# Kernel optimization log

Hardware: AMD Instinct MI355X
Metric: run time of the kernel (lower is better)

## Reference

```python
import jax, jax.numpy as jnp
import numpy as np

B, S, H = 4, 2048, 512
E, K = 8, 2
DFF = 4 * H


def setup_inputs() -> dict:
    key = jax.random.key(0)
    ks = jax.random.split(key, 6)
    x = jax.random.normal(ks[0], (B, S, H), dtype=jnp.float32)
    gate_W = jax.random.normal(ks[1], (H, E), dtype=jnp.float32) * 0.02
    gate_b = jnp.zeros((E,), dtype=jnp.float32)
    # Stacked expert params; Linear stored as [in, out] so y = x @ W + b
    W1 = jax.random.normal(ks[2], (E, H, DFF), dtype=jnp.float32) * 0.02
    b1 = jnp.zeros((E, DFF), dtype=jnp.float32)
    W2 = jax.random.normal(ks[3], (E, DFF, H), dtype=jnp.float32) * 0.02
    b2 = jnp.zeros((E, H), dtype=jnp.float32)
    return {"x": x, "gate_W": gate_W, "gate_b": gate_b,
            "W1": W1, "b1": b1, "W2": W2, "b2": b2}


def reference(x, gate_W, gate_b, W1, b1, W2, b2):
    bsz, seq, hid = x.shape
    flat = x.reshape(-1, hid)                       # [T, H]
    T = flat.shape[0]
    gate_logits = flat @ gate_W + gate_b            # [T, E]
    topk_vals, topk_idx = jax.lax.top_k(gate_logits, K)   # [T, K]
    topk_w = jax.nn.softmax(topk_vals, axis=-1)      # softmax over selected logits only

    # Scatter top-k weights into a dense per-token combine matrix [T, E];
    # zero weight where a token is not routed -> identical math to masked dispatch.
    combine = jnp.zeros((T, E), dtype=flat.dtype).at[
        jnp.arange(T)[:, None], topk_idx].add(topk_w)

    out_flat = jnp.zeros_like(flat)
    for e in range(E):  # fixed small loop over structurally distinct experts
        h = jax.nn.gelu(flat @ W1[e] + b1[e], approximate=False) @ W2[e] + b2[e]
        out_flat = out_flat + h * combine[:, e:e + 1]
    out = out_flat.reshape(bsz, seq, hid)

    probs = jax.nn.softmax(gate_logits, axis=-1).mean(axis=0)   # [E]
    l_aux = jnp.sum(probs * probs) * E
    expert_counts = jnp.zeros((E,), dtype=jnp.float32).at[
        topk_idx.reshape(-1)].add(1.0)
    return out, l_aux, expert_counts
```

## Files before the change

kernel.cpp:

```cpp
#include <hip/hip_runtime.h>
#include <math.h>

#define TOK 8192
#define HD  512
#define NE  8
#define DFF 2048

typedef __attribute__((ext_vector_type(8))) short bf16x8;
typedef __attribute__((ext_vector_type(4))) float floatx4;

__device__ inline unsigned short f2bf(float f) {
    union { float f; unsigned u; } v; v.f = f;
    unsigned r = v.u + 0x7FFFu + ((v.u >> 16) & 1u);
    return (unsigned short)(r >> 16);
}

__device__ inline float gelu_exact(float v) {
    return 0.5f * v * (1.f + erff(v * 0.70710678118654752f));
}

typedef __attribute__((address_space(1))) const unsigned int glb_u32;
typedef __attribute__((address_space(3))) unsigned int lds_u32;
__device__ __forceinline__ void gload16(const unsigned short* g, unsigned short* l) {
    __builtin_amdgcn_global_load_lds((glb_u32*)g, (lds_u32*)l, 16, 0, 0);
}

__global__ __launch_bounds__(256) void prep_kernel(
    const float* __restrict__ x, const float* __restrict__ gW, const float* __restrict__ gb,
    const float* __restrict__ W1, const float* __restrict__ W2,
    int* __restrict__ seg_count, float* __restrict__ probs_sum,
    int* __restrict__ seg_token, float* __restrict__ seg_w,
    unsigned short* __restrict__ xb,
    unsigned short* __restrict__ W1t, unsigned short* __restrict__ W2t)
{
    __shared__ __align__(16) char shraw[16896];
    int bid = blockIdx.x;
    int tid = threadIdx.x;

    if (bid >= 32) {
        int b = bid - 32;
        float (*tile)[65] = (float(*)[65])shraw;
        int z = b >> 8, rem = b & 255;
        int xq = rem & 31, yq = rem >> 5;
        const float* src; unsigned short* dst; int C, R, cb, rb;
        if (z < NE) {
            src = W1 + (size_t)z * HD * DFF; dst = W1t + (size_t)z * HD * DFF;
            R = HD; C = DFF; cb = xq; rb = yq;
        } else {
            int e = z - NE;
            src = W2 + (size_t)e * DFF * HD; dst = W2t + (size_t)e * DFF * HD;
            R = DFF; C = HD; cb = yq; rb = xq;
        }
        int c0 = cb * 64, r0 = rb * 64;
        int lc = tid & 63, lrw = tid >> 6;
        #pragma unroll
        for (int rr = lrw; rr < 64; rr += 4)
            tile[rr][lc] = src[(size_t)(r0 + rr) * C + c0 + lc];
        __syncthreads();
        #pragma unroll
        for (int cc = lrw; cc < 64; cc += 4)
            dst[(size_t)(c0 + cc) * R + r0 + lc] = f2bf(tile[lc][cc]);
        return;
    }

    float* sW    = (float*)shraw;
    float* psum  = (float*)(shraw + 16384);
    int*   lcount = (int*)(shraw + 16448);
    int*   lbase  = (int*)(shraw + 16512);

    for (int i = tid; i < HD * NE; i += 256) sW[i] = gW[i];
    if (tid < NE) { psum[tid] = 0.f; lcount[tid] = 0; }
    __syncthreads();

    int t = bid * 256 + tid;
    float logit[NE];
    #pragma unroll
    for (int e = 0; e < NE; e++) logit[e] = gb[e];

    const float4* xr4 = reinterpret_cast<const float4*>(x + (size_t)t * HD);
    ushort4* xbw = reinterpret_cast<ushort4*>(xb + (size_t)t * HD);
    for (int j4 = 0; j4 < HD / 4; j4++) {
        float4 xv = xr4[j4];
        int j = j4 * 4;
        ushort4 o; o.x = f2bf(xv.x); o.y = f2bf(xv.y); o.z = f2bf(xv.z); o.w = f2bf(xv.w);
        xbw[j4] = o;
        #pragma unroll
        for (int e = 0; e < NE; e++) {
            logit[e] += xv.x * sW[(j + 0) * NE + e] + xv.y * sW[(j + 1) * NE + e]
                      + xv.z * sW[(j + 2) * NE + e] + xv.w * sW[(j + 3) * NE + e];
        }
    }

    float mx = logit[0];
    #pragma unroll
    for (int e = 1; e < NE; e++) mx = fmaxf(mx, logit[e]);
    float pe[NE]; float s = 0.f;
    #pragma unroll
    for (int e = 0; e < NE; e++) { pe[e] = expf(logit[e] - mx); s += pe[e]; }
    float inv = 1.f / s;
    int l = tid & 63;
    #pragma unroll
    for (int e = 0; e < NE; e++) {
        float v = pe[e] * inv;
        for (int off = 32; off; off >>= 1) v += __shfl_down(v, off);
        if (l == 0) atomicAdd(&psum[e], v);
    }

    int i0 = 0; float v0 = logit[0];
    #pragma unroll
    for (int e = 1; e < NE; e++) if (logit[e] > v0) { v0 = logit[e]; i0 = e; }
    int i1 = -1; float v1 = -3.4e38f;
    #pragma unroll
    for (int e = 0; e < NE; e++) if (e != i0 && logit[e] > v1) { v1 = logit[e]; i1 = e; }
    float e1 = expf(v1 - v0);
    float w0 = 1.f / (1.f + e1);
    float w1 = e1 / (1.f + e1);

    int r0 = atomicAdd(&lcount[i0], 1);
    int r1 = atomicAdd(&lcount[i1], 1);
    __syncthreads();
    if (tid < NE) lbase[tid] = atomicAdd(&seg_count[tid], lcount[tid]);
    __syncthreads();
    int p0 = lbase[i0] + r0;
    seg_token[i0 * TOK + p0] = t; seg_w[i0 * TOK + p0] = w0;
    int p1 = lbase[i1] + r1;
    seg_token[i1 * TOK + p1] = t; seg_w[i1 * TOK + p1] = w1;

    __syncthreads();
    if (tid < NE) atomicAdd(&probs_sum[tid], psum[tid]);
}

#define TM  128
#define TN  128
#define BK  32

__global__ __launch_bounds__(256) void gemm1_kernel(
    const unsigned short* __restrict__ xb,
    const unsigned short* __restrict__ W1t,
    const float* __restrict__ bias1,
    const int* __restrict__ seg_count, const float* __restrict__ probs_sum,
    const int* __restrict__ seg_token,
    unsigned short* __restrict__ hbuf,
    float* __restrict__ out_tail)
{
    int bid = blockIdx.x;
    int tid = threadIdx.x;

    if (bid == 0) {
        if (tid < NE) out_tail[1 + tid] = (float)seg_count[tid];
        else if (tid == 64) {
            float s = 0.f;
            #pragma unroll
            for (int e2 = 0; e2 < NE; e2++) {
                float p = probs_sum[e2] * (1.f / (float)TOK);
                s += p * p;
            }
            out_tail[0] = s * (float)NE;
        }
    }

    int e  = bid & 7;
    int r2 = bid >> 3;
    int nb = r2 & 15;
    int mb = r2 >> 4;
    int cnt = seg_count[e];
    if (mb * TM >= cnt) return;
    int off_e = 0;
    #pragma unroll
    for (int ee = 0; ee < NE; ee++) if (ee < e) off_e += (seg_count[ee] + 127) & ~127;
    int hb = off_e + mb * TM;

    __shared__ __align__(16) unsigned short smem[3][2][TM * BK];
    __shared__ int tok_s[TM];
    if (tid < TM) {
        int gi = mb * TM + tid;
        tok_s[tid] = seg_token[e * TOK + ((gi < cnt) ? gi : 0)];
    }
    __syncthreads();

    int w = tid >> 6, l = tid & 63;
    int lr = l & 15, crow = (l >> 4) * 4;
    int wm = (w & 1) * 64, wn = (w >> 1) * 64;
    int kq = (l >> 4) * 8;
    const unsigned short* w1e = W1t + (size_t)e * DFF * HD + (size_t)(nb * TN) * HD;

    unsigned aofs[2], bofs[2];
    #pragma unroll
    for (int s = 0; s < 2; s++) {
        int r = w * 32 + s * 16 + (l >> 2);
        aofs[s] = (unsigned)tok_s[r] * HD + (unsigned)((l & 3) * 8);
        bofs[s] = (unsigned)(r * HD) + (unsigned)((l & 3) * 8);
    }

    floatx4 acc[4][4];
    #pragma unroll
    for (int i = 0; i < 4; i++)
        #pragma unroll
        for (int j = 0; j < 4; j++) acc[i][j] = (floatx4){0.f, 0.f, 0.f, 0.f};

    #pragma unroll
    for (int p = 0; p < 2; p++)
        #pragma unroll
        for (int s = 0; s < 2; s++) {
            gload16(xb  + aofs[s] + p * BK, &smem[p][0][(w * 32 + s * 16) * BK]);
            gload16(w1e + bofs[s] + p * BK, &smem[p][1][(w * 32 + s * 16) * BK]);
        }

    const int NIT = HD / BK;
    int rb = 0;
    for (int k = 0; k < NIT; ++k) {
        if (k + 1 < NIT) asm volatile("s_waitcnt vmcnt(4)" ::: "memory");
        else             asm volatile("s_waitcnt vmcnt(0)" ::: "memory");
        __builtin_amdgcn_s_barrier();
        asm volatile("" ::: "memory");
        if (k + 2 < NIT) {
            int ib = (rb == 0) ? 2 : rb - 1;
            int ko = (k + 2) * BK;
            #pragma unroll
            for (int s = 0; s < 2; s++) {
                gload16(xb  + aofs[s] + ko, &smem[ib][0][(w * 32 + s * 16) * BK]);
                gload16(w1e + bofs[s] + ko, &smem[ib][1][(w * 32 + s * 16) * BK]);
            }
        }
        const unsigned short* A = smem[rb][0];
        const unsigned short* B = smem[rb][1];
        bf16x8 a[4], b[4];
        #pragma unroll
        for (int i = 0; i < 4; i++) a[i] = *(const bf16x8*)&A[(wm + 16 * i + lr) * BK + kq];
        #pragma unroll
        for (int j = 0; j < 4; j++) b[j] = *(const bf16x8*)&B[(wn + 16 * j + lr) * BK + kq];
        __builtin_amdgcn_s_setprio(1);
        #pragma unroll
        for (int i = 0; i < 4; i++)
            #pragma unroll
            for (int j = 0; j < 4; j++)
                acc[i][j] = __builtin_amdgcn_mfma_f32_16x16x32_bf16(a[i], b[j], acc[i][j], 0, 0, 0);
        __builtin_amdgcn_s_setprio(0);
        rb = (rb == 2) ? 0 : rb + 1;
    }
    __syncthreads();

    unsigned short* scr = &smem[0][0][0] + w * 64 * 72;
    #pragma unroll
    for (int j = 0; j < 4; j++) {
        float b1v = bias1[e * DFF + nb * TN + wn + 16 * j + lr];
        #pragma unroll
        for (int i = 0; i < 4; i++)
            #pragma unroll
            for (int rr = 0; rr < 4; rr++)
                scr[(16 * i + crow + rr) * 72 + 16 * j + lr] = f2bf(gelu_exact(acc[i][j][rr] + b1v));
    }
    __syncthreads();
    int lh = l >> 3, ll = l & 7;
    #pragma unroll
    for (int k = 0; k < 8; k++) {
        uint4 v = *(const uint4*)&scr[(8 * k + lh) * 72 + ll * 8];
        int grow = hb + wm + 8 * k + lh;
        *(uint4*)&hbuf[(size_t)grow * DFF + nb * TN + wn + ll * 8] = v;
    }
}

__global__ __launch_bounds__(256) void gemm2_kernel(
    const unsigned short* __restrict__ hbuf,
    const unsigned short* __restrict__ W2t,
    const float* __restrict__ b2,
    const int* __restrict__ seg_count, const int* __restrict__ seg_token,
    const float* __restrict__ seg_w,
    float* __restrict__ out)
{
    int bid = blockIdx.x;
    int tid = threadIdx.x;
    int e  = bid & 7;
    int r2 = bid >> 3;
    int nb = r2 & 3;
    int mb = r2 >> 2;
    int cnt = seg_count[e];
    if (mb * TM >= cnt) return;
    int off_e = 0;
    #pragma unroll
    for (int ee = 0; ee < NE; ee++) if (ee < e) off_e += (seg_count[ee] + 127) & ~127;
    int hb = off_e + mb * TM;

    __shared__ __align__(16) unsigned short smem[3][2][TM * BK];
    __shared__ int   tok_s[TM];
    __shared__ float wgt_s[TM];
    if (tid < TM) {
        int gi = mb * TM + tid;
        tok_s[tid] = seg_token[e * TOK + ((gi < cnt) ? gi : 0)];
        wgt_s[tid] = (gi < cnt) ? seg_w[e * TOK + gi] : 0.f;
    }
    __syncthreads();

    int w = tid >> 6, l = tid & 63;
    int lr = l & 15, crow = (l >> 4) * 4;
    int wm = (w & 1) * 64, wn = (w >> 1) * 64;
    int kq = (l >> 4) * 8;
    const unsigned short* w2e = W2t + (size_t)e * HD * DFF + (size_t)(nb * TN) * DFF;

    unsigned aofs[2], bofs[2];
    #pragma unroll
    for (int s = 0; s < 2; s++) {
        int r = w * 32 + s * 16 + (l >> 2);
        aofs[s] = (unsigned)((hb + r) * DFF) + (unsigned)((l & 3) * 8);
        bofs[s] = (unsigned)(r * DFF) + (unsigned)((l & 3) * 8);
    }

    floatx4 acc[4][4];
    #pragma unroll
    for (int i = 0; i < 4; i++)
        #pragma unroll
        for (int j = 0; j < 4; j++) acc[i][j] = (floatx4){0.f, 0.f, 0.f, 0.f};

    #pragma unroll
    for (int p = 0; p < 2; p++)
        #pragma unroll
        for (int s = 0; s < 2; s++) {
            gload16(hbuf + aofs[s] + p * BK, &smem[p][0][(w * 32 + s * 16) * BK]);
            gload16(w2e  + bofs[s] + p * BK, &smem[p][1][(w * 32 + s * 16) * BK]);
        }

    const int NIT = DFF / BK;
    int rb = 0;
    for (int k = 0; k < NIT; ++k) {
        if (k + 1 < NIT) asm volatile("s_waitcnt vmcnt(4)" ::: "memory");
        else             asm volatile("s_waitcnt vmcnt(0)" ::: "memory");
        __builtin_amdgcn_s_barrier();
        asm volatile("" ::: "memory");
        if (k + 2 < NIT) {
            int ib = (rb == 0) ? 2 : rb - 1;
            int ko = (k + 2) * BK;
            #pragma unroll
            for (int s = 0; s < 2; s++) {
                gload16(hbuf + aofs[s] + ko, &smem[ib][0][(w * 32 + s * 16) * BK]);
                gload16(w2e  + bofs[s] + ko, &smem[ib][1][(w * 32 + s * 16) * BK]);
            }
        }
        const unsigned short* A = smem[rb][0];
        const unsigned short* B = smem[rb][1];
        bf16x8 a[4], b[4];
        #pragma unroll
        for (int i = 0; i < 4; i++) a[i] = *(const bf16x8*)&A[(wm + 16 * i + lr) * BK + kq];
        #pragma unroll
        for (int j = 0; j < 4; j++) b[j] = *(const bf16x8*)&B[(wn + 16 * j + lr) * BK + kq];
        __builtin_amdgcn_s_setprio(1);
        #pragma unroll
        for (int i = 0; i < 4; i++)
            #pragma unroll
            for (int j = 0; j < 4; j++)
                acc[i][j] = __builtin_amdgcn_mfma_f32_16x16x32_bf16(a[i], b[j], acc[i][j], 0, 0, 0);
        __builtin_amdgcn_s_setprio(0);
        rb = (rb == 2) ? 0 : rb + 1;
    }

    #pragma unroll
    for (int j = 0; j < 4; j++) {
        int n = nb * TN + wn + 16 * j + lr;
        float b2v = b2[e * HD + n];
        #pragma unroll
        for (int i = 0; i < 4; i++)
            #pragma unroll
            for (int rr = 0; rr < 4; rr++) {
                int m = wm + 16 * i + crow + rr;
                atomicAdd(&out[(size_t)tok_s[m] * HD + n], (acc[i][j][rr] + b2v) * wgt_s[m]);
            }
    }
}

#define BMT 64
#define FK  64
#define XS_LD 520
#define HS_LD 72

__global__ __launch_bounds__(256, 2) void ffn_fused_fallback(
    const unsigned short* __restrict__ xb,
    const unsigned short* __restrict__ W1t, const float* __restrict__ b1,
    const unsigned short* __restrict__ W2t, const float* __restrict__ b2,
    const int* __restrict__ seg_count, const int* __restrict__ seg_token,
    const float* __restrict__ seg_w, float* __restrict__ out)
{
    int bid = blockIdx.x;
    int e = bid & 7;
    int g = bid >> 3;
    int cnt = seg_count[e];
    int n0 = g * BMT;
    if (n0 >= cnt) return;
    int rows = min(BMT, cnt - n0);

    __shared__ unsigned short xs[BMT * XS_LD];
    __shared__ unsigned short hs[BMT * HS_LD];
    __shared__ int   tok_s[BMT];
    __shared__ float wgt_s[BMT];

    int tid = threadIdx.x;
    if (tid < BMT) {
        int idx = (tid < rows) ? (n0 + tid) : n0;
        tok_s[tid] = seg_token[e * TOK + idx];
        wgt_s[tid] = (tid < rows) ? seg_w[e * TOK + idx] : 0.f;
    }
    __syncthreads();
    {
        int r = tid >> 2, q = tid & 3;
        const uint4* src = (const uint4*)(xb + (size_t)tok_s[r] * HD) + q * 16;
        uint4* dst = (uint4*)&xs[(size_t)r * XS_LD + q * 128];
        #pragma unroll
        for (int i = 0; i < 16; i++) dst[i] = src[i];
    }
    __syncthreads();

    int w = tid >> 6, l = tid & 63;
    int lr = l & 15, lk = (l >> 4) * 8, crow = (l >> 4) * 4;

    const unsigned short* w1e = W1t + (size_t)e * DFF * HD;
    const unsigned short* w2e = W2t + (size_t)e * HD * DFF;

    floatx4 acc2[4][8];
    #pragma unroll
    for (int i = 0; i < 4; i++)
        #pragma unroll
        for (int j = 0; j < 8; j++) acc2[i][j] = (floatx4){0.f, 0.f, 0.f, 0.f};

    for (int fc = 0; fc < DFF; fc += FK) {
        floatx4 acc1[4];
        #pragma unroll
        for (int t = 0; t < 4; t++) acc1[t] = (floatx4){0.f, 0.f, 0.f, 0.f};
        const unsigned short* w1c = w1e + (size_t)fc * HD;
        for (int ks = 0; ks < HD; ks += 32) {
            bf16x8 a = *(const bf16x8*)&xs[(16 * w + lr) * XS_LD + ks + lk];
            #pragma unroll
            for (int t = 0; t < 4; t++) {
                bf16x8 b = *(const bf16x8*)(w1c + (size_t)(16 * t + lr) * HD + ks + lk);
                acc1[t] = __builtin_amdgcn_mfma_f32_16x16x32_bf16(a, b, acc1[t], 0, 0, 0);
            }
        }
        __syncthreads();
        #pragma unroll
        for (int t = 0; t < 4; t++) {
            float b1v = b1[e * DFF + fc + 16 * t + lr];
            #pragma unroll
            for (int r = 0; r < 4; r++)
                hs[(16 * w + crow + r) * HS_LD + 16 * t + lr] = f2bf(gelu_exact(acc1[t][r] + b1v));
        }
        __syncthreads();
        #pragma unroll
        for (int ks = 0; ks < FK; ks += 32) {
            bf16x8 af[4];
            #pragma unroll
            for (int i = 0; i < 4; i++) af[i] = *(const bf16x8*)&hs[(16 * i + lr) * HS_LD + ks + lk];
            #pragma unroll 4
            for (int j = 0; j < 8; j++) {
                bf16x8 b = *(const bf16x8*)(w2e + (size_t)(128 * w + 16 * j + lr) * DFF + fc + ks + lk);
                #pragma unroll
                for (int i = 0; i < 4; i++)
                    acc2[i][j] = __builtin_amdgcn_mfma_f32_16x16x32_bf16(af[i], b, acc2[i][j], 0, 0, 0);
            }
        }
    }
    #pragma unroll
    for (int j = 0; j < 8; j++) {
        int n = 128 * w + 16 * j + lr;
        float b2v = b2[e * HD + n];
        #pragma unroll
        for (int i = 0; i < 4; i++)
            #pragma unroll
            for (int r = 0; r < 4; r++) {
                int m = 16 * i + crow + r;
                atomicAdd(&out[(size_t)tok_s[m] * HD + n], (acc2[i][j][r] + b2v) * wgt_s[m]);
            }
    }
}

__global__ void finalize_kernel(const int* __restrict__ seg_count,
                                const float* __restrict__ probs_sum,
                                float* __restrict__ out_tail)
{
    int tid = threadIdx.x;
    if (tid < NE) out_tail[1 + tid] = (float)seg_count[tid];
    if (tid == 0) {
        float s = 0.f;
        #pragma unroll
        for (int e = 0; e < NE; e++) {
            float p = probs_sum[e] * (1.f / (float)TOK);
            s += p * p;
        }
        out_tail[0] = s * (float)NE;
    }
}

extern "C" void kernel_launch(void* const* d_in, const int* in_sizes, int n_in,
                              void* d_out, int out_size, void* d_ws, size_t ws_size,
                              hipStream_t stream)
{
    const float* x  = (const float*)d_in[0];
    const float* gW = (const float*)d_in[1];
    const float* gb = (const float*)d_in[2];
    const float* W1 = (const float*)d_in[3];
    const float* b1 = (const float*)d_in[4];
    const float* W2 = (const float*)d_in[5];
    const float* b2 = (const float*)d_in[6];
    float* out = (float*)d_out;

    char* ws = (char*)d_ws;
    int*   seg_count = (int*)ws;
    float* probs_sum = (float*)(ws + 32);
    int*   seg_token = (int*)(ws + 262144);
    float* seg_w     = (float*)(ws + 262144 + (size_t)NE * TOK * 4);
    unsigned short* xb   = (unsigned short*)(ws + (1u  << 20));
    unsigned short* W1t  = (unsigned short*)(ws + (16u << 20));
    unsigned short* W2t  = (unsigned short*)(ws + (32u << 20));
    unsigned short* hbuf = (unsigned short*)(ws + (48u << 20));

    const size_t WS_SPLIT = (size_t)(48u << 20) + (size_t)17408 * DFF * 2;

    hipMemsetAsync(d_ws, 0, 64, stream);
    hipMemsetAsync(d_out, 0, (size_t)TOK * HD * sizeof(float), stream);

    prep_kernel<<<4128, 256, 0, stream>>>(x, gW, gb, W1, W2,
                                          seg_count, probs_sum, seg_token, seg_w,
                                          xb, W1t, W2t);

    if (ws_size >= WS_SPLIT) {
        gemm1_kernel<<<NE * (DFF / TN) * 64, 256, 0, stream>>>(
            xb, W1t, b1, seg_count, probs_sum, seg_token, hbuf,
            out + (size_t)TOK * HD);
        gemm2_kernel<<<NE * (HD / TN) * 64, 256, 0, stream>>>(
            hbuf, W2t, b2, seg_count, seg_token, seg_w, out);
    } else {
        finalize_kernel<<<1, 64, 0, stream>>>(seg_count, probs_sum, out + (size_t)TOK * HD);
        ffn_fused_fallback<<<(TOK / BMT) * NE, 256, 0, stream>>>(
            xb, W1t, b1, W2t, b2, seg_count, seg_token, seg_w, out);
    }
}
```

Measured before the change: 349.6 us.

## Use 8-wave blocks, XOR-swizzled LDS, and split-K for expert GEMMs

Both expert GEMM kernels now launch 512 threads per 128x128 tile, so each wave owns a 64x32 sub-tile and issues one async load per operand per stage instead of two. A 16-byte XOR swizzle on the global-to-LDS column offsets and the fragment reads is meant to cut LDS bank conflicts. The second GEMM splits its K dimension in half across two blocks that both atomically accumulate into the output, with the bias added only by the first half. The aim is more latency hiding and more blocks for the long K loop, at the cost of twice the atomic traffic on the output and a less synchronized gemm1 epilogue, which now relies on each wave reading back only its own scratch region.

```diff
diff --git a/kernel.cpp b/kernel.cpp
--- a/kernel.cpp
+++ b/kernel.cpp
@@ -134,7 +134,7 @@
 #define TN  128
 #define BK  32
 
-__global__ __launch_bounds__(256) void gemm1_kernel(
+__global__ __launch_bounds__(512, 5) void gemm1_kernel(
     const unsigned short* __restrict__ xb,
     const unsigned short* __restrict__ W1t,
     const float* __restrict__ bias1,
@@ -180,87 +180,78 @@
 
     int w = tid >> 6, l = tid & 63;
     int lr = l & 15, crow = (l >> 4) * 4;
-    int wm = (w & 1) * 64, wn = (w >> 1) * 64;
-    int kq = (l >> 4) * 8;
+    int wm = (w & 1) * 64, wn = (w >> 1) * 32;
+    int rsw = ((l >> 4) ^ ((lr >> 1) & 3)) * 8;
     const unsigned short* w1e = W1t + (size_t)e * DFF * HD + (size_t)(nb * TN) * HD;
 
-    unsigned aofs[2], bofs[2];
-    #pragma unroll
-    for (int s = 0; s < 2; s++) {
-        int r = w * 32 + s * 16 + (l >> 2);
-        aofs[s] = (unsigned)tok_s[r] * HD + (unsigned)((l & 3) * 8);
-        bofs[s] = (unsigned)(r * HD) + (unsigned)((l & 3) * 8);
-    }
-
-    floatx4 acc[4][4];
+    int sr = w * 16 + (l >> 2);
+    unsigned csrc = (unsigned)(((l & 3) ^ ((l >> 3) & 3)) * 8);
+    unsigned aofs = (unsigned)tok_s[sr] * HD + csrc;
+    unsigned bofs = (unsigned)sr * HD + csrc;
+
+    floatx4 acc[4][2];
     #pragma unroll
     for (int i = 0; i < 4; i++)
         #pragma unroll
-        for (int j = 0; j < 4; j++) acc[i][j] = (floatx4){0.f, 0.f, 0.f, 0.f};
-
-    #pragma unroll
-    for (int p = 0; p < 2; p++)
-        #pragma unroll
-        for (int s = 0; s < 2; s++) {
-            gload16(xb  + aofs[s] + p * BK, &smem[p][0][(w * 32 + s * 16) * BK]);
-            gload16(w1e + bofs[s] + p * BK, &smem[p][1][(w * 32 + s * 16) * BK]);
-        }
+        for (int j = 0; j < 2; j++) acc[i][j] = (floatx4){0.f, 0.f, 0.f, 0.f};
+
+    #pragma unroll
+    for (int p = 0; p < 2; p++) {
+        gload16(xb  + aofs + p * BK, &smem[p][0][(w * 16) * BK]);
+        gload16(w1e + bofs + p * BK, &smem[p][1][(w * 16) * BK]);
+    }
 
     const int NIT = HD / BK;
     int rb = 0;
     for (int k = 0; k < NIT; ++k) {
-        if (k + 1 < NIT) asm volatile("s_waitcnt vmcnt(4)" ::: "memory");
+        if (k + 1 < NIT) asm volatile("s_waitcnt vmcnt(2)" ::: "memory");
         else             asm volatile("s_waitcnt vmcnt(0)" ::: "memory");
         __builtin_amdgcn_s_barrier();
         asm volatile("" ::: "memory");
         if (k + 2 < NIT) {
             int ib = (rb == 0) ? 2 : rb - 1;
             int ko = (k + 2) * BK;
-            #pragma unroll
-            for (int s = 0; s < 2; s++) {
-                gload16(xb  + aofs[s] + ko, &smem[ib][0][(w * 32 + s * 16) * BK]);
-                gload16(w1e + bofs[s] + ko, &smem[ib][1][(w * 32 + s * 16) * BK]);
-            }
+            gload16(xb  + aofs + ko, &smem[ib][0][(w * 16) * BK]);
+            gload16(w1e + bofs + ko, &smem[ib][1][(w * 16) * BK]);
         }
         const unsigned short* A = smem[rb][0];
         const unsigned short* B = smem[rb][1];
-        bf16x8 a[4], b[4];
-        #pragma unroll
-        for (int i = 0; i < 4; i++) a[i] = *(const bf16x8*)&A[(wm + 16 * i + lr) * BK + kq];
-        #pragma unroll
-        for (int j = 0; j < 4; j++) b[j] = *(const bf16x8*)&B[(wn + 16 * j + lr) * BK + kq];
+        bf16x8 a[4], b[2];
+        #pragma unroll
+        for (int i = 0; i < 4; i++) a[i] = *(const bf16x8*)&A[(wm + 16 * i + lr) * BK + rsw];
+        #pragma unroll
+        for (int j = 0; j < 2; j++) b[j] = *(const bf16x8*)&B[(wn + 16 * j + lr) * BK + rsw];
         __builtin_amdgcn_s_setprio(1);
         #pragma unroll
         for (int i = 0; i < 4; i++)
             #pragma unroll
-            for (int j = 0; j < 4; j++)
+            for (int j = 0; j < 2; j++)
                 acc[i][j] = __builtin_amdgcn_mfma_f32_16x16x32_bf16(a[i], b[j], acc[i][j], 0, 0, 0);
         __builtin_amdgcn_s_setprio(0);
         rb = (rb == 2) ? 0 : rb + 1;
     }
     __syncthreads();
 
-    unsigned short* scr = &smem[0][0][0] + w * 64 * 72;
-    #pragma unroll
-    for (int j = 0; j < 4; j++) {
+    unsigned short* scr = &smem[0][0][0] + w * (64 * 40);
+    #pragma unroll
+    for (int j = 0; j < 2; j++) {
         float b1v = bias1[e * DFF + nb * TN + wn + 16 * j + lr];
         #pragma unroll
         for (int i = 0; i < 4; i++)
             #pragma unroll
             for (int rr = 0; rr < 4; rr++)
-                scr[(16 * i + crow + rr) * 72 + 16 * j + lr] = f2bf(gelu_exact(acc[i][j][rr] + b1v));
-    }
-    __syncthreads();
-    int lh = l >> 3, ll = l & 7;
-    #pragma unroll
-    for (int k = 0; k < 8; k++) {
-        uint4 v = *(const uint4*)&scr[(8 * k + lh) * 72 + ll * 8];
-        int grow = hb + wm + 8 * k + lh;
-        *(uint4*)&hbuf[(size_t)grow * DFF + nb * TN + wn + ll * 8] = v;
-    }
-}
-
-__global__ __launch_bounds__(256) void gemm2_kernel(
+                scr[(16 * i + crow + rr) * 40 + 16 * j + lr] = f2bf(gelu_exact(acc[i][j][rr] + b1v));
+    }
+    int rq = l >> 2, cq = l & 3;
+    #pragma unroll
+    for (int kk = 0; kk < 4; kk++) {
+        uint4 v = *(const uint4*)&scr[(kk * 16 + rq) * 40 + cq * 8];
+        int grow = hb + wm + kk * 16 + rq;
+        *(uint4*)&hbuf[(size_t)grow * DFF + nb * TN + wn + cq * 8] = v;
+    }
+}
+
+__global__ __launch_bounds__(512, 5) void gemm2_kernel(
     const unsigned short* __restrict__ hbuf,
     const unsigned short* __restrict__ W2t,
     const float* __restrict__ b2,
@@ -271,9 +262,10 @@
     int bid = blockIdx.x;
     int tid = threadIdx.x;
     int e  = bid & 7;
-    int r2 = bid >> 3;
-    int nb = r2 & 3;
-    int mb = r2 >> 2;
+    int t2 = bid >> 3;
+    int kh = t2 & 1;
+    int nb = (t2 >> 1) & 3;
+    int mb = t2 >> 3;
     int cnt = seg_count[e];
     if (mb * TM >= cnt) return;
     int off_e = 0;
@@ -293,69 +285,62 @@
 
     int w = tid >> 6, l = tid & 63;
     int lr = l & 15, crow = (l >> 4) * 4;
-    int wm = (w & 1) * 64, wn = (w >> 1) * 64;
-    int kq = (l >> 4) * 8;
+    int wm = (w & 1) * 64, wn = (w >> 1) * 32;
+    int rsw = ((l >> 4) ^ ((lr >> 1) & 3)) * 8;
     const unsigned short* w2e = W2t + (size_t)e * HD * DFF + (size_t)(nb * TN) * DFF;
 
-    unsigned aofs[2], bofs[2];
-    #pragma unroll
-    for (int s = 0; s < 2; s++) {
-        int r = w * 32 + s * 16 + (l >> 2);
-        aofs[s] = (unsigned)((hb + r) * DFF) + (unsigned)((l & 3) * 8);
-        bofs[s] = (unsigned)(r * DFF) + (unsigned)((l & 3) * 8);
-    }
-
-    floatx4 acc[4][4];
+    int sr = w * 16 + (l >> 2);
+    unsigned csrc = (unsigned)(((l & 3) ^ ((l >> 3) & 3)) * 8);
+    unsigned kbase = (unsigned)kh * (DFF / 2);
+    unsigned aofs = (unsigned)(hb + sr) * DFF + kbase + csrc;
+    unsigned bofs = (unsigned)sr * DFF + kbase + csrc;
+
+    floatx4 acc[4][2];
     #pragma unroll
     for (int i = 0; i < 4; i++)
         #pragma unroll
-        for (int j = 0; j < 4; j++) acc[i][j] = (floatx4){0.f, 0.f, 0.f, 0.f};
-
-    #pragma unroll
-    for (int p = 0; p < 2; p++)
-        #pragma unroll
-        for (int s = 0; s < 2; s++) {
-            gload16(hbuf + aofs[s] + p * BK, &smem[p][0][(w * 32 + s * 16) * BK]);
-            gload16(w2e  + bofs[s] + p * BK, &smem[p][1][(w * 32 + s * 16) * BK]);
-        }
-
-    const int NIT = DFF / BK;
+        for (int j = 0; j < 2; j++) acc[i][j] = (floatx4){0.f, 0.f, 0.f, 0.f};
+
+    #pragma unroll
+    for (int p = 0; p < 2; p++) {
+        gload16(hbuf + aofs + p * BK, &smem[p][0][(w * 16) * BK]);
+        gload16(w2e  + bofs + p * BK, &smem[p][1][(w * 16) * BK]);
+    }
+
+    const int NIT = (DFF / 2) / BK;
     int rb = 0;
     for (int k = 0; k < NIT; ++k) {
-        if (k + 1 < NIT) asm volatile("s_waitcnt vmcnt(4)" ::: "memory");
+        if (k + 1 < NIT) asm volatile("s_waitcnt vmcnt(2)" ::: "memory");
         else             asm volatile("s_waitcnt vmcnt(0)" ::: "memory");
         __builtin_amdgcn_s_barrier();
         asm volatile("" ::: "memory");
         if (k + 2 < NIT) {
             int ib = (rb == 0) ? 2 : rb - 1;
             int ko = (k + 2) * BK;
-            #pragma unroll
-            for (int s = 0; s < 2; s++) {
-                gload16(hbuf + aofs[s] + ko, &smem[ib][0][(w * 32 + s * 16) * BK]);
-                gload16(w2e  + bofs[s] + ko, &smem[ib][1][(w * 32 + s * 16) * BK]);
-            }
+            gload16(hbuf + aofs + ko, &smem[ib][0][(w * 16) * BK]);
+            gload16(w2e  + bofs + ko, &smem[ib][1][(w * 16) * BK]);
         }
         const unsigned short* A = smem[rb][0];
         const unsigned short* B = smem[rb][1];
-        bf16x8 a[4], b[4];
-        #pragma unroll
-        for (int i = 0; i < 4; i++) a[i] = *(const bf16x8*)&A[(wm + 16 * i + lr) * BK + kq];
-        #pragma unroll
-        for (int j = 0; j < 4; j++) b[j] = *(const bf16x8*)&B[(wn + 16 * j + lr) * BK + kq];
+        bf16x8 a[4], b[2];
+        #pragma unroll
+        for (int i = 0; i < 4; i++) a[i] = *(const bf16x8*)&A[(wm + 16 * i + lr) * BK + rsw];
+        #pragma unroll
+        for (int j = 0; j < 2; j++) b[j] = *(const bf16x8*)&B[(wn + 16 * j + lr) * BK + rsw];
         __builtin_amdgcn_s_setprio(1);
         #pragma unroll
         for (int i = 0; i < 4; i++)
             #pragma unroll
-            for (int j = 0; j < 4; j++)
+            for (int j = 0; j < 2; j++)
                 acc[i][j] = __builtin_amdgcn_mfma_f32_16x16x32_bf16(a[i], b[j], acc[i][j], 0, 0, 0);
         __builtin_amdgcn_s_setprio(0);
         rb = (rb == 2) ? 0 : rb + 1;
     }
 
     #pragma unroll
-    for (int j = 0; j < 4; j++) {
+    for (int j = 0; j < 2; j++) {
         int n = nb * TN + wn + 16 * j + lr;
-        float b2v = b2[e * HD + n];
+        float b2v = (kh == 0) ? b2[e * HD + n] : 0.f;
         #pragma unroll
         for (int i = 0; i < 4; i++)
             #pragma unroll
@@ -519,10 +504,10 @@
                                           xb, W1t, W2t);
 
     if (ws_size >= WS_SPLIT) {
-        gemm1_kernel<<<NE * (DFF / TN) * 64, 256, 0, stream>>>(
+        gemm1_kernel<<<NE * (DFF / TN) * 64, 512, 0, stream>>>(
             xb, W1t, b1, seg_count, probs_sum, seg_token, hbuf,
             out + (size_t)TOK * HD);
-        gemm2_kernel<<<NE * (HD / TN) * 64, 256, 0, stream>>>(
+        gemm2_kernel<<<NE * (HD / TN) * 2 * 64, 512, 0, stream>>>(
             hbuf, W2t, b2, seg_count, seg_token, seg_w, out);
     } else {
         finalize_kernel<<<1, 64, 0, stream>>>(seg_count, probs_sum, out + (size_t)TOK * HD);
```

New measurement: 371.7 us. 6.3% more time.

## Replace output atomics with per-rank partial buffer and swizzle LDS tiles

Applied to the files above, without the earlier changes.

Tags each routed token entry with its top-k rank and has the second GEMM write weighted expert outputs to a per-token, per-rank partial buffer instead of using float atomicAdd on the output. A small combine kernel then sums the two partials into the output, which also removes the output memset on this path. The GEMM kernels additionally XOR-swizzle the 16-byte chunk placement in LDS to reduce bank conflicts on fragment reads. It costs an extra 32MB buffer round trip, adds a workspace-size branch, and relies on token ids fitting in 16 bits.

```diff
diff --git a/kernel.cpp b/kernel.cpp
--- a/kernel.cpp
+++ b/kernel.cpp
@@ -122,9 +122,11 @@
     if (tid < NE) lbase[tid] = atomicAdd(&seg_count[tid], lcount[tid]);
     __syncthreads();
     int p0 = lbase[i0] + r0;
-    seg_token[i0 * TOK + p0] = t; seg_w[i0 * TOK + p0] = w0;
+    seg_token[i0 * TOK + p0] = t;
+    seg_w[i0 * TOK + p0] = w0;
     int p1 = lbase[i1] + r1;
-    seg_token[i1 * TOK + p1] = t; seg_w[i1 * TOK + p1] = w1;
+    seg_token[i1 * TOK + p1] = t | (1 << 16);
+    seg_w[i1 * TOK + p1] = w1;
 
     __syncthreads();
     if (tid < NE) atomicAdd(&probs_sum[tid], psum[tid]);
@@ -174,22 +176,23 @@
     __shared__ int tok_s[TM];
     if (tid < TM) {
         int gi = mb * TM + tid;
-        tok_s[tid] = seg_token[e * TOK + ((gi < cnt) ? gi : 0)];
+        tok_s[tid] = seg_token[e * TOK + ((gi < cnt) ? gi : 0)] & 0xFFFF;
     }
     __syncthreads();
 
     int w = tid >> 6, l = tid & 63;
     int lr = l & 15, crow = (l >> 4) * 4;
     int wm = (w & 1) * 64, wn = (w >> 1) * 64;
-    int kq = (l >> 4) * 8;
+    int rsw = ((l >> 4) ^ ((lr >> 1) & 3)) * 8;
     const unsigned short* w1e = W1t + (size_t)e * DFF * HD + (size_t)(nb * TN) * HD;
 
+    unsigned csrc = (unsigned)(((l & 3) ^ ((l >> 3) & 3)) * 8);
     unsigned aofs[2], bofs[2];
     #pragma unroll
     for (int s = 0; s < 2; s++) {
         int r = w * 32 + s * 16 + (l >> 2);
-        aofs[s] = (unsigned)tok_s[r] * HD + (unsigned)((l & 3) * 8);
-        bofs[s] = (unsigned)(r * HD) + (unsigned)((l & 3) * 8);
+        aofs[s] = (unsigned)tok_s[r] * HD + csrc;
+        bofs[s] = (unsigned)(r * HD) + csrc;
     }
 
     floatx4 acc[4][4];
@@ -226,9 +229,9 @@
         const unsigned short* B = smem[rb][1];
         bf16x8 a[4], b[4];
         #pragma unroll
-        for (int i = 0; i < 4; i++) a[i] = *(const bf16x8*)&A[(wm + 16 * i + lr) * BK + kq];
-        #pragma unroll
-        for (int j = 0; j < 4; j++) b[j] = *(const bf16x8*)&B[(wn + 16 * j + lr) * BK + kq];
+        for (int i = 0; i < 4; i++) a[i] = *(const bf16x8*)&A[(wm + 16 * i + lr) * BK + rsw];
+        #pragma unroll
+        for (int j = 0; j < 4; j++) b[j] = *(const bf16x8*)&B[(wn + 16 * j + lr) * BK + rsw];
         __builtin_amdgcn_s_setprio(1);
         #pragma unroll
         for (int i = 0; i < 4; i++)
@@ -266,7 +269,9 @@
     const float* __restrict__ b2,
     const int* __restrict__ seg_count, const int* __restrict__ seg_token,
     const float* __restrict__ seg_w,
-    float* __restrict__ out)
+    float* __restrict__ pout,
+    float* __restrict__ out,
+    int use_pout)
 {
     int bid = blockIdx.x;
     int tid = threadIdx.x;
@@ -283,10 +288,13 @@
 
     __shared__ __align__(16) unsigned short smem[3][2][TM * BK];
     __shared__ int   tok_s[TM];
+    __shared__ int   rnk_s[TM];
     __shared__ float wgt_s[TM];
     if (tid < TM) {
         int gi = mb * TM + tid;
-        tok_s[tid] = seg_token[e * TOK + ((gi < cnt) ? gi : 0)];
+        int raw = seg_token[e * TOK + ((gi < cnt) ? gi : 0)];
+        tok_s[tid] = raw & 0xFFFF;
+        rnk_s[tid] = raw >> 16;
         wgt_s[tid] = (gi < cnt) ? seg_w[e * TOK + gi] : 0.f;
     }
     __syncthreads();
@@ -294,15 +302,16 @@
     int w = tid >> 6, l = tid & 63;
     int lr = l & 15, crow = (l >> 4) * 4;
     int wm = (w & 1) * 64, wn = (w >> 1) * 64;
-    int kq = (l >> 4) * 8;
+    int rsw = ((l >> 4) ^ ((lr >> 1) & 3)) * 8;
     const unsigned short* w2e = W2t + (size_t)e * HD * DFF + (size_t)(nb * TN) * DFF;
 
+    unsigned csrc = (unsigned)(((l & 3) ^ ((l >> 3) & 3)) * 8);
     unsigned aofs[2], bofs[2];
     #pragma unroll
     for (int s = 0; s < 2; s++) {
         int r = w * 32 + s * 16 + (l >> 2);
-        aofs[s] = (unsigned)((hb + r) * DFF) + (unsigned)((l & 3) * 8);
-        bofs[s] = (unsigned)(r * DFF) + (unsigned)((l & 3) * 8);
+        aofs[s] = (unsigned)((hb + r) * DFF) + csrc;
+        bofs[s] = (unsigned)(r * DFF) + csrc;
     }
 
     floatx4 acc[4][4];
@@ -339,9 +348,9 @@
         const unsigned short* B = smem[rb][1];
         bf16x8 a[4], b[4];
         #pragma unroll
-        for (int i = 0; i < 4; i++) a[i] = *(const bf16x8*)&A[(wm + 16 * i + lr) * BK + kq];
-        #pragma unroll
-        for (int j = 0; j < 4; j++) b[j] = *(const bf16x8*)&B[(wn + 16 * j + lr) * BK + kq];
+        for (int i = 0; i < 4; i++) a[i] = *(const bf16x8*)&A[(wm + 16 * i + lr) * BK + rsw];
+        #pragma unroll
+        for (int j = 0; j < 4; j++) b[j] = *(const bf16x8*)&B[(wn + 16 * j + lr) * BK + rsw];
         __builtin_amdgcn_s_setprio(1);
         #pragma unroll
         for (int i = 0; i < 4; i++)
@@ -352,18 +361,48 @@
         rb = (rb == 2) ? 0 : rb + 1;
     }
 
-    #pragma unroll
-    for (int j = 0; j < 4; j++) {
-        int n = nb * TN + wn + 16 * j + lr;
-        float b2v = b2[e * HD + n];
-        #pragma unroll
-        for (int i = 0; i < 4; i++)
-            #pragma unroll
-            for (int rr = 0; rr < 4; rr++) {
-                int m = wm + 16 * i + crow + rr;
-                atomicAdd(&out[(size_t)tok_s[m] * HD + n], (acc[i][j][rr] + b2v) * wgt_s[m]);
-            }
-    }
+    if (use_pout) {
+        #pragma unroll
+        for (int j = 0; j < 4; j++) {
+            int n = nb * TN + wn + 16 * j + lr;
+            float b2v = b2[e * HD + n];
+            #pragma unroll
+            for (int i = 0; i < 4; i++)
+                #pragma unroll
+                for (int rr = 0; rr < 4; rr++) {
+                    int m = wm + 16 * i + crow + rr;
+                    if (mb * TM + m < cnt)
+                        pout[((size_t)tok_s[m] * 2 + rnk_s[m]) * HD + n] =
+                            (acc[i][j][rr] + b2v) * wgt_s[m];
+                }
+        }
+    } else {
+        #pragma unroll
+        for (int j = 0; j < 4; j++) {
+            int n = nb * TN + wn + 16 * j + lr;
+            float b2v = b2[e * HD + n];
+            #pragma unroll
+            for (int i = 0; i < 4; i++)
+                #pragma unroll
+                for (int rr = 0; rr < 4; rr++) {
+                    int m = wm + 16 * i + crow + rr;
+                    atomicAdd(&out[(size_t)tok_s[m] * HD + n], (acc[i][j][rr] + b2v) * wgt_s[m]);
+                }
+        }
+    }
+}
+
+__global__ __launch_bounds__(256) void combine_kernel(
+    const float* __restrict__ pout, float* __restrict__ out)
+{
+    int idx = blockIdx.x * 256 + threadIdx.x;
+    int t = idx >> 7;
+    int c4 = idx & 127;
+    const float4* p = (const float4*)pout;
+    float4 a = p[((size_t)t * 2 + 0) * 128 + c4];
+    float4 b = p[((size_t)t * 2 + 1) * 128 + c4];
+    float4 r; r.x = a.x + b.x; r.y = a.y + b.y; r.z = a.z + b.z; r.w = a.w + b.w;
+    ((float4*)out)[idx] = r;
 }
 
 #define BMT 64
@@ -394,7 +433,7 @@
     int tid = threadIdx.x;
     if (tid < BMT) {
         int idx = (tid < rows) ? (n0 + tid) : n0;
-        tok_s[tid] = seg_token[e * TOK + idx];
+        tok_s[tid] = seg_token[e * TOK + idx] & 0xFFFF;
         wgt_s[tid] = (tid < rows) ? seg_w[e * TOK + idx] : 0.f;
     }
     __syncthreads();
@@ -502,29 +541,66 @@
     char* ws = (char*)d_ws;
     int*   seg_count = (int*)ws;
     float* probs_sum = (float*)(ws + 32);
-    int*   seg_token = (int*)(ws + 262144);
-    float* seg_w     = (float*)(ws + 262144 + (size_t)NE * TOK * 4);
-    unsigned short* xb   = (unsigned short*)(ws + (1u  << 20));
-    unsigned short* W1t  = (unsigned short*)(ws + (16u << 20));
-    unsigned short* W2t  = (unsigned short*)(ws + (32u << 20));
-    unsigned short* hbuf = (unsigned short*)(ws + (48u << 20));
-
-    const size_t WS_SPLIT = (size_t)(48u << 20) + (size_t)17408 * DFF * 2;
+    int*   seg_token = (int*)(ws + 4096);
+    float* seg_w     = (float*)(ws + 4096 + (size_t)NE * TOK * 4);
+
+    const size_t HBUF_BYTES = (size_t)17408 * DFF * 2;
+
+    const size_t F_POUT = 0xA0000;
+    const size_t F_XB   = (1u  << 20);
+    const size_t F_W1T  = (9u  << 20);
+    const size_t F_W2T  = F_POUT + (size_t)TOK * 2 * HD * 4;
+    const size_t F_HBUF = F_W2T + ((size_t)NE * DFF * HD * 2);
+    const size_t WS_FAST = F_HBUF + HBUF_BYTES;
+
+    const size_t M_XB   = (1u  << 20);
+    const size_t M_W1T  = (16u << 20);
+    const size_t M_W2T  = (32u << 20);
+    const size_t M_HBUF = (48u << 20);
+    const size_t WS_MID = M_HBUF + HBUF_BYTES;
 
     hipMemsetAsync(d_ws, 0, 64, stream);
-    hipMemsetAsync(d_out, 0, (size_t)TOK * HD * sizeof(float), stream);
-
-    prep_kernel<<<4128, 256, 0, stream>>>(x, gW, gb, W1, W2,
-                                          seg_count, probs_sum, seg_token, seg_w,
-                                          xb, W1t, W2t);
-
-    if (ws_size >= WS_SPLIT) {
+
+    if (ws_size >= WS_FAST) {
+        unsigned short* xb   = (unsigned short*)(ws + F_XB);
+        unsigned short* W1t  = (unsigned short*)(ws + F_W1T);
+        unsigned short* W2t  = (unsigned short*)(ws + F_W2T);
+        unsigned short* hbuf = (unsigned short*)(ws + F_HBUF);
+        float*          pout = (float*)(ws + F_POUT);
+
+        prep_kernel<<<4128, 256, 0, stream>>>(x, gW, gb, W1, W2,
+                                              seg_count, probs_sum, seg_token, seg_w,
+                                              xb, W1t, W2t);
         gemm1_kernel<<<NE * (DFF / TN) * 64, 256, 0, stream>>>(
             xb, W1t, b1, seg_count, probs_sum, seg_token, hbuf,
             out + (size_t)TOK * HD);
         gemm2_kernel<<<NE * (HD / TN) * 64, 256, 0, stream>>>(
-            hbuf, W2t, b2, seg_count, seg_token, seg_w, out);
+            hbuf, W2t, b2, seg_count, seg_token, seg_w, pout, out, 1);
+        combine_kernel<<<(TOK * HD / 4) / 256, 256, 0, stream>>>(pout, out);
+    } else if (ws_size >= WS_MID) {
+        unsigned short* xb   = (unsigned short*)(ws + M_XB);
+        unsigned short* W1t  = (unsigned short*)(ws + M_W1T);
+        unsigned short* W2t  = (unsigned short*)(ws + M_W2T);
+        unsigned short* hbuf = (unsigned short*)(ws + M_HBUF);
+
+        hipMemsetAsync(d_out, 0, (size_t)TOK * HD * sizeof(float), stream);
+        prep_kernel<<<4128, 256, 0, stream>>>(x, gW, gb, W1, W2,
+                                              seg_count, probs_sum, seg_token, seg_w,
+                                              xb, W1t, W2t);
+        gemm1_kernel<<<NE * (DFF / TN) * 64, 256, 0, stream>>>(
+            xb, W1t, b1, seg_count, probs_sum, seg_token, hbuf,
+            out + (size_t)TOK * HD);
+        gemm2_kernel<<<NE * (HD / TN) * 64, 256, 0, stream>>>(
+            hbuf, W2t, b2, seg_count, seg_token, seg_w, (float*)ws, out, 0);
     } else {
+        unsigned short* xb   = (unsigned short*)(ws + M_XB);
+        unsigned short* W1t  = (unsigned short*)(ws + M_W1T);
+        unsigned short* W2t  = (unsigned short*)(ws + M_W2T);
+
+        hipMemsetAsync(d_out, 0, (size_t)TOK * HD * sizeof(float), stream);
+        prep_kernel<<<4128, 256, 0, stream>>>(x, gW, gb, W1, W2,
+                                              seg_count, probs_sum, seg_token, seg_w,
+                                              xb, W1t, W2t);
         finalize_kernel<<<1, 64, 0, stream>>>(seg_count, probs_sum, out + (size_t)TOK * HD);
         ffn_fused_fallback<<<(TOK / BMT) * NE, 256, 0, stream>>>(
             xb, W1t, b1, W2t, b2, seg_count, seg_token, seg_w, out);
```

New measurement: 354.8 us. Within noise of the previous version (+1.5%).
